# Performance work log

Hardware: AMD Instinct MI355X
Metric: run time of the kernel (lower is better)

The kernel has to match this reference:

```python
import jax, jax.numpy as jnp
import numpy as np

B, T = 32, 128
V, E, H = 32000, 512, 1024
SOS_IDX = 1


def setup_inputs() -> dict:
    key = jax.random.key(0)
    ks = jax.random.split(key, 9)
    s = lambda n: 1.0 / np.sqrt(n)
    return {
        "target": jax.random.randint(ks[0], (B, T), 0, V, dtype=jnp.int64),
        "h0": jax.random.normal(ks[1], (B, H), dtype=jnp.float32),
        "emb": jax.random.normal(ks[2], (V, E), dtype=jnp.float32),
        "W_ih": jax.random.normal(ks[3], (H, E), dtype=jnp.float32) * s(E),
        "b_ih": jax.random.normal(ks[4], (H,), dtype=jnp.float32) * s(E),
        "W_hh": jax.random.normal(ks[5], (H, H), dtype=jnp.float32) * s(H),
        "b_hh": jax.random.normal(ks[6], (H,), dtype=jnp.float32) * s(H),
        "W_out": jax.random.normal(ks[7], (V, H), dtype=jnp.float32) * s(H),
        "b_out": jax.random.normal(ks[8], (V,), dtype=jnp.float32) * s(H),
    }


def reference(target, h0, emb, W_ih, b_ih, W_hh, b_hh, W_out, b_out):
    # Teacher-forcing ratio fixed at 1.0 (deterministic): input tokens are
    # [sos, target[:,1], ..., target[:,T-1]] per the original `target[:, t+1]`.
    Bb, Tt = target.shape
    sos = jnp.full((Bb, 1), SOS_IDX, dtype=target.dtype)
    tokens = jnp.concatenate([sos, target[:, 1:]], axis=1)  # (B, T)
    x = emb[tokens]  # (B, T, E) -- embedding gather done once, vectorized

    def step(h, x_t):
        # manual RNN cell: h' = tanh(x W_ih^T + b_ih + h W_hh^T + b_hh)
        h = jnp.tanh(x_t @ W_ih.T + b_ih + h @ W_hh.T + b_hh)  # (B, H)
        out = h @ W_out.T + b_out  # (B, V) linear decode
        return h, out

    _, outs = jax.lax.scan(step, h0, jnp.swapaxes(x, 0, 1))  # (T, B, V)
    return jnp.swapaxes(outs, 0, 1)  # (B, T, V)
```

## Files before the change

kernel.cpp:

```cpp
#include <hip/hip_runtime.h>
#include <stdint.h>

#define T_SEQ 128
#define B_SZ  32
#define H_DIM 1024
#define E_DIM 512
#define V_DIM 32000
#define SOS_TOK 1
#define NCONS 224
#define NTILES 8000

typedef float v4f __attribute__((ext_vector_type(4)));
typedef short short8 __attribute__((ext_vector_type(8)));

__device__ inline uint16_t f2bf(float x) {
    uint32_t u = __float_as_uint(x);
    uint32_t r = (u + 0x7fffu + ((u >> 16) & 1u)) >> 16;
    return (uint16_t)r;
}
__device__ inline uint32_t pack2(float a, float b) {
    return (uint32_t)f2bf(a) | ((uint32_t)f2bf(b) << 16);
}

__device__ inline void gload16(const void* g, void* l) {
    __builtin_amdgcn_global_load_lds(
        (const __attribute__((address_space(1))) uint32_t*)g,
        (__attribute__((address_space(3))) uint32_t*)l, 16, 0, 0);
}

__global__ __launch_bounds__(256) void kconv(const float* __restrict__ W,
                                             uint16_t* __restrict__ Wb) {
    size_t i = ((size_t)blockIdx.x * 256 + threadIdx.x) * 8;
    float4 a = *(const float4*)&W[i];
    float4 c = *(const float4*)&W[i + 4];
    uint4 p;
    p.x = pack2(a.x, a.y); p.y = pack2(a.z, a.w);
    p.z = pack2(c.x, c.y); p.w = pack2(c.z, c.w);
    *(uint4*)&Wb[i] = p;
}

__global__ __launch_bounds__(256) void kxwm(const int* __restrict__ target,
                                            const float* __restrict__ emb,
                                            const float* __restrict__ Wih,
                                            const float* __restrict__ bih,
                                            const float* __restrict__ bhh,
                                            float* __restrict__ xW) {
    __shared__ __align__(16) uint16_t As[128 * 32];
    __shared__ __align__(16) uint16_t Bs[128 * 32];
    __shared__ int toks[128];
    int m0 = blockIdx.x * 128, n0 = blockIdx.y * 128;
    int tid = threadIdx.x;
    if (tid < 128) {
        int row = m0 + tid;
        int t = row & (T_SEQ - 1);
        toks[tid] = (t == 0) ? SOS_TOK : target[row];
    }
    __syncthreads();

    v4f acc[4][4] = {};
    int lane = tid & 63, wv = tid >> 6, wm = wv >> 1, wn = wv & 1;
    int ar = lane & 15, ko = (lane >> 4) * 8;

    for (int k0 = 0; k0 < E_DIM; k0 += 32) {
#pragma unroll
        for (int l = 0; l < 2; ++l) {
            int c = tid + l * 256;
            int r = c >> 2, ko8 = (c & 3) * 8;
            const float* asrc = &emb[(size_t)toks[r] * E_DIM + k0 + ko8];
            float4 x = *(const float4*)asrc;
            float4 y = *(const float4*)(asrc + 4);
            uint4 p;
            p.x = pack2(x.x, x.y); p.y = pack2(x.z, x.w);
            p.z = pack2(y.x, y.y); p.w = pack2(y.z, y.w);
            *(uint4*)&As[r * 32 + ko8] = p;
            const float* bsrc = &Wih[(size_t)(n0 + r) * E_DIM + k0 + ko8];
            float4 u = *(const float4*)bsrc;
            float4 v = *(const float4*)(bsrc + 4);
            uint4 q;
            q.x = pack2(u.x, u.y); q.y = pack2(u.z, u.w);
            q.z = pack2(v.x, v.y); q.w = pack2(v.z, v.w);
            *(uint4*)&Bs[r * 32 + ko8] = q;
        }
        __syncthreads();

        short8 a[4], bfr[4];
#pragma unroll
        for (int i = 0; i < 4; ++i)
            a[i] = *(const short8*)&As[(wm * 64 + i * 16 + ar) * 32 + ko];
#pragma unroll
        for (int jj = 0; jj < 4; ++jj)
            bfr[jj] = *(const short8*)&Bs[(wn * 64 + jj * 16 + ar) * 32 + ko];
#pragma unroll
        for (int i = 0; i < 4; ++i)
#pragma unroll
            for (int jj = 0; jj < 4; ++jj)
                acc[i][jj] = __builtin_amdgcn_mfma_f32_16x16x32_bf16(
                    a[i], bfr[jj], acc[i][jj], 0, 0, 0);
        __syncthreads();
    }

    int fr = lane & 15, fq = lane >> 4;
#pragma unroll
    for (int jj = 0; jj < 4; ++jj) {
        int col = n0 + wn * 64 + jj * 16 + fr;
        float bias = bih[col] + bhh[col];
#pragma unroll
        for (int i = 0; i < 4; ++i) {
            int row = m0 + wm * 64 + i * 16 + fq * 4;
#pragma unroll
            for (int q = 0; q < 4; ++q) {
                int m = row + q;
                int b = m >> 7, t = m & (T_SEQ - 1);
                xW[((size_t)t * B_SZ + b) * H_DIM + col] = acc[i][jj][q] + bias;
            }
        }
    }
}

template <bool BBF>
__global__ __launch_bounds__(256) void kfused(const uint16_t* __restrict__ hbInit,
                                              const uint16_t* __restrict__ WbHH,
                                              const float* __restrict__ xW,
                                              uint16_t* __restrict__ Hb,
                                              uint32_t* __restrict__ flags,
                                              const void* __restrict__ Bop,
                                              const float* __restrict__ bout,
                                              float* __restrict__ out) {
    __shared__ __align__(16) uint16_t As[128 * 32];
    __shared__ __align__(16) uint16_t Bs[128 * 32];
    int tid = threadIdx.x;
    int lane = tid & 63;

    if (blockIdx.x < 32) {
        __builtin_amdgcn_s_setprio(1);
        int blk = blockIdx.x;
        int bg = blk & 1, ngg = blk >> 1;
        int w = tid >> 6;
        int ncol0 = ngg * 64 + w * 16;
        int lr = lane & 15, lk = (lane >> 4) * 8;

        short8 wf[32];
        const uint16_t* wrow = WbHH + (size_t)(ncol0 + lr) * H_DIM + lk;
#pragma unroll
        for (int kt = 0; kt < 32; ++kt)
            wf[kt] = *(const short8*)(wrow + (size_t)kt * 32);

        int brow = bg * 16 + lr;
        int eb = bg * 16 + (lane >> 4) * 4;
        int en = ncol0 + lr;
        uint32_t* Hb32 = (uint32_t*)Hb;
        uint32_t* myflag = flags + (size_t)(bg * 16 + ngg) * 32;
        const uint32_t* grpflags = flags + (size_t)(bg * 16) * 32;

        for (int t = 0; t < T_SEQ; ++t) {
            const uint16_t* arow =
                ((t == 0) ? hbInit : Hb + (size_t)(t - 1) * B_SZ * H_DIM)
                + (size_t)brow * H_DIM + lk;

            float xv[4];
#pragma unroll
            for (int q = 0; q < 4; ++q)
                xv[q] = xW[((size_t)t * B_SZ + eb + q) * H_DIM + en];

            v4f ac0 = {0.f,0.f,0.f,0.f}, ac1 = {0.f,0.f,0.f,0.f};
            v4f ac2 = {0.f,0.f,0.f,0.f}, ac3 = {0.f,0.f,0.f,0.f};
            short8 af0[16], af1[16];
#pragma unroll
            for (int kt = 0; kt < 16; ++kt)
                af0[kt] = *(const short8*)(arow + (size_t)kt * 32);
#pragma unroll
            for (int kt = 0; kt < 16; ++kt)
                af1[kt] = *(const short8*)(arow + 512 + (size_t)kt * 32);
#pragma unroll
            for (int kt = 0; kt < 16; ++kt) {
                v4f* a = (kt & 3) == 0 ? &ac0 : (kt & 3) == 1 ? &ac1
                        : (kt & 3) == 2 ? &ac2 : &ac3;
                *a = __builtin_amdgcn_mfma_f32_16x16x32_bf16(af0[kt], wf[kt], *a, 0, 0, 0);
            }
#pragma unroll
            for (int kt = 0; kt < 16; ++kt) {
                v4f* a = (kt & 3) == 0 ? &ac0 : (kt & 3) == 1 ? &ac1
                        : (kt & 3) == 2 ? &ac2 : &ac3;
                *a = __builtin_amdgcn_mfma_f32_16x16x32_bf16(af1[kt], wf[16 + kt], *a, 0, 0, 0);
            }
            v4f acc = (ac0 + ac1) + (ac2 + ac3);

            float hv[4];
#pragma unroll
            for (int q = 0; q < 4; ++q)
                hv[q] = tanhf(acc[q] + xv[q]);

#pragma unroll
            for (int q = 0; q < 4; ++q) {
                float pv = __shfl_xor(hv[q], 1);
                bool mine = ((lane & 1) == 0) ? (q < 2) : (q >= 2);
                if (mine) {
                    uint32_t word = (lane & 1) ? pack2(pv, hv[q]) : pack2(hv[q], pv);
                    size_t i32 = (((size_t)t * B_SZ + eb + q) * H_DIM
                                  + (size_t)(en & ~1)) >> 1;
                    __hip_atomic_store(&Hb32[i32], word, __ATOMIC_RELAXED,
                                       __HIP_MEMORY_SCOPE_AGENT);
                }
            }

            __syncthreads();
            if (tid == 0)
                __hip_atomic_store(myflag, (uint32_t)(t + 1), __ATOMIC_RELEASE,
                                   __HIP_MEMORY_SCOPE_AGENT);
            if (t < T_SEQ - 1) {
                if (tid < 16) {
                    const uint32_t* f = grpflags + (size_t)tid * 32;
                    while (__hip_atomic_load(f, __ATOMIC_RELAXED,
                                             __HIP_MEMORY_SCOPE_AGENT) <= (uint32_t)t)
                        __builtin_amdgcn_s_sleep(2);
                }
                if (tid == 0)
                    (void)__hip_atomic_load(myflag, __ATOMIC_ACQUIRE,
                                            __HIP_MEMORY_SCOPE_AGENT);
                __syncthreads();
            }
        }
    } else {
        int c = blockIdx.x - 32;
        int wv = tid >> 6, wm = wv >> 1, wn = wv & 1;
        int ar = lane & 15, ko = (lane >> 4) * 8;
        int sx = BBF ? (((ar >> 1) & 3) << 3) : 0;
        int fr = lane & 15, fq = lane >> 4;
        int gate_seen = 0;
        const uint32_t* proxyf = flags + (size_t)(c & 31) * 32;

        const uint16_t* Bb = (const uint16_t*)Bop;
        const float*    Bf = (const float*)Bop;

        for (int g = c; g < NTILES; g += NCONS) {
            int mtp = g / 250, nt = g - mtp * 250;
            int need = 4 * mtp + 4;
            if (need > gate_seen) {
                if (tid == 0) {
                    while (__hip_atomic_load(proxyf, __ATOMIC_RELAXED,
                                             __HIP_MEMORY_SCOPE_AGENT) < (uint32_t)need)
                        __builtin_amdgcn_s_sleep(32);
                }
                __syncthreads();
                if (tid < 32) {
                    const uint32_t* f = flags + (size_t)tid * 32;
                    while (__hip_atomic_load(f, __ATOMIC_RELAXED,
                                             __HIP_MEMORY_SCOPE_AGENT) < (uint32_t)need)
                        __builtin_amdgcn_s_sleep(2);
                }
                __syncthreads();
                if (tid == 0)
                    (void)__hip_atomic_load(flags, __ATOMIC_ACQUIRE,
                                            __HIP_MEMORY_SCOPE_AGENT);
                __syncthreads();
                gate_seen = need;
            }

            int m0 = mtp * 128, n0 = nt * 128;
            v4f acc[4][4] = {};

            for (int k0 = 0; k0 < H_DIM; k0 += 32) {
                int wb = tid & ~63;
                if constexpr (BBF) {
#pragma unroll
                    for (int l = 0; l < 2; ++l) {
                        int cc = tid + l * 256;
                        int r = cc >> 2;
                        int gsw = ((cc & 3) ^ ((cc >> 3) & 3)) * 8;
                        gload16(&Hb[(size_t)(m0 + r) * H_DIM + k0 + gsw],
                                (char*)As + (size_t)(wb + l * 256) * 16);
                        gload16(&Bb[(size_t)(n0 + r) * H_DIM + k0 + gsw],
                                (char*)Bs + (size_t)(wb + l * 256) * 16);
                    }
                } else {
#pragma unroll
                    for (int l = 0; l < 2; ++l) {
                        int cc = tid + l * 256;
                        int r = cc >> 2, ko8 = (cc & 3) * 8;
                        gload16(&Hb[(size_t)(m0 + r) * H_DIM + k0 + ko8],
                                (char*)As + (size_t)(wb + l * 256) * 16);
                        const float* src = &Bf[(size_t)(n0 + r) * H_DIM + k0 + ko8];
                        float4 x = *(const float4*)src;
                        float4 y = *(const float4*)(src + 4);
                        uint4 p;
                        p.x = pack2(x.x, x.y); p.y = pack2(x.z, x.w);
                        p.z = pack2(y.x, y.y); p.w = pack2(y.z, y.w);
                        *(uint4*)&Bs[r * 32 + ko8] = p;
                    }
                }
                __syncthreads();

                short8 a[4], bfr[4];
#pragma unroll
                for (int i = 0; i < 4; ++i)
                    a[i] = *(const short8*)&As[(wm * 64 + i * 16 + ar) * 32 + (ko ^ sx)];
#pragma unroll
                for (int jj = 0; jj < 4; ++jj)
                    bfr[jj] = *(const short8*)&Bs[(wn * 64 + jj * 16 + ar) * 32 + (ko ^ sx)];
#pragma unroll
                for (int i = 0; i < 4; ++i)
#pragma unroll
                    for (int jj = 0; jj < 4; ++jj)
                        acc[i][jj] = __builtin_amdgcn_mfma_f32_16x16x32_bf16(
                            a[i], bfr[jj], acc[i][jj], 0, 0, 0);
                __syncthreads();
            }

#pragma unroll
            for (int jj = 0; jj < 4; ++jj) {
                int col = n0 + wn * 64 + jj * 16 + fr;
                float bo = bout[col];
#pragma unroll
                for (int i = 0; i < 4; ++i) {
                    int rbase = wm * 64 + i * 16 + fq * 4;
#pragma unroll
                    for (int q = 0; q < 4; ++q) {
                        int mp = m0 + rbase + q;
                        int tt = mp >> 5, bb = mp & 31;
                        out[((size_t)bb * T_SEQ + tt) * V_DIM + col] =
                            acc[i][jj][q] + bo;
                    }
                }
            }
        }
    }
}

extern "C" void kernel_launch(void* const* d_in, const int* in_sizes, int n_in,
                              void* d_out, int out_size, void* d_ws, size_t ws_size,
                              hipStream_t stream) {
    const int*   target = (const int*)d_in[0];
    const float* h0     = (const float*)d_in[1];
    const float* emb    = (const float*)d_in[2];
    const float* Wih    = (const float*)d_in[3];
    const float* bih    = (const float*)d_in[4];
    const float* Whh    = (const float*)d_in[5];
    const float* bhh    = (const float*)d_in[6];
    const float* Wout   = (const float*)d_in[7];
    const float* bout   = (const float*)d_in[8];
    float* out = (float*)d_out;

    char* ws = (char*)d_ws;
    float*    xW     = (float*)(ws);
    uint16_t* WbHH   = (uint16_t*)(ws + 16777216);
    uint16_t* hbInit = (uint16_t*)(ws + 18874368);
    uint32_t* flags  = (uint32_t*)(ws + 18939904);
    uint16_t* Hb     = (uint16_t*)(ws + 18944000);
    uint16_t* WbOut  = (uint16_t*)(ws + 27332608);
    const bool wbok = ws_size >= 92868608ull;

    kconv<<<512, 256, 0, stream>>>(Whh, WbHH);
    kconv<<<16, 256, 0, stream>>>(h0, hbInit);
    kxwm<<<dim3(32, 8), 256, 0, stream>>>(target, emb, Wih, bih, bhh, xW);
    hipMemsetAsync(flags, 0, 4096, stream);

    if (wbok) {
        kconv<<<16000, 256, 0, stream>>>(Wout, WbOut);
        kfused<true><<<32 + NCONS, 256, 0, stream>>>(hbInit, WbHH, xW, Hb, flags,
                                                     (const void*)WbOut, bout, out);
    } else {
        kfused<false><<<32 + NCONS, 256, 0, stream>>>(hbInit, WbHH, xW, Hb, flags,
                                                      (const void*)Wout, bout, out);
    }
}
```

Baseline: 1.069 ms.

## Fold weight bf16 conversions into fused kernel to overlap with recurrence

Removes the separate conversion kernels for W_hh, h0 and W_out. The recurrence blocks now convert W_hh and h0 to bf16 in registers on load, and the consumer blocks convert W_out into the workspace at kernel start, then wait on an atomic counter barrier before the output GEMM tiles. The W_out conversion can then run while the early recurrence steps execute, and fewer kernels are launched. The cost is a grid-wide spin barrier among the consumer blocks, which assumes all of them are resident at once.

```diff
diff --git a/kernel.cpp b/kernel.cpp
--- a/kernel.cpp
+++ b/kernel.cpp
@@ -9,6 +9,7 @@
 #define SOS_TOK 1
 #define NCONS 224
 #define NTILES 8000
+#define NGRAN 4096000
 
 typedef float v4f __attribute__((ext_vector_type(4)));
 typedef short short8 __attribute__((ext_vector_type(8)));
@@ -21,22 +22,19 @@
 __device__ inline uint32_t pack2(float a, float b) {
     return (uint32_t)f2bf(a) | ((uint32_t)f2bf(b) << 16);
 }
+__device__ inline short8 packf8(const float* p) {
+    float4 x = *(const float4*)p;
+    float4 y = *(const float4*)(p + 4);
+    uint4 v;
+    v.x = pack2(x.x, x.y); v.y = pack2(x.z, x.w);
+    v.z = pack2(y.x, y.y); v.w = pack2(y.z, y.w);
+    return *(short8*)&v;
+}
 
 __device__ inline void gload16(const void* g, void* l) {
     __builtin_amdgcn_global_load_lds(
         (const __attribute__((address_space(1))) uint32_t*)g,
         (__attribute__((address_space(3))) uint32_t*)l, 16, 0, 0);
-}
-
-__global__ __launch_bounds__(256) void kconv(const float* __restrict__ W,
-                                             uint16_t* __restrict__ Wb) {
-    size_t i = ((size_t)blockIdx.x * 256 + threadIdx.x) * 8;
-    float4 a = *(const float4*)&W[i];
-    float4 c = *(const float4*)&W[i + 4];
-    uint4 p;
-    p.x = pack2(a.x, a.y); p.y = pack2(a.z, a.w);
-    p.z = pack2(c.x, c.y); p.w = pack2(c.z, c.w);
-    *(uint4*)&Wb[i] = p;
 }
 
 __global__ __launch_bounds__(256) void kxwm(const int* __restrict__ target,
@@ -66,20 +64,10 @@
         for (int l = 0; l < 2; ++l) {
             int c = tid + l * 256;
             int r = c >> 2, ko8 = (c & 3) * 8;
-            const float* asrc = &emb[(size_t)toks[r] * E_DIM + k0 + ko8];
-            float4 x = *(const float4*)asrc;
-            float4 y = *(const float4*)(asrc + 4);
-            uint4 p;
-            p.x = pack2(x.x, x.y); p.y = pack2(x.z, x.w);
-            p.z = pack2(y.x, y.y); p.w = pack2(y.z, y.w);
-            *(uint4*)&As[r * 32 + ko8] = p;
-            const float* bsrc = &Wih[(size_t)(n0 + r) * E_DIM + k0 + ko8];
-            float4 u = *(const float4*)bsrc;
-            float4 v = *(const float4*)(bsrc + 4);
-            uint4 q;
-            q.x = pack2(u.x, u.y); q.y = pack2(u.z, u.w);
-            q.z = pack2(v.x, v.y); q.w = pack2(v.z, v.w);
-            *(uint4*)&Bs[r * 32 + ko8] = q;
+            short8 av = packf8(&emb[(size_t)toks[r] * E_DIM + k0 + ko8]);
+            short8 bv = packf8(&Wih[(size_t)(n0 + r) * E_DIM + k0 + ko8]);
+            *(short8*)&As[r * 32 + ko8] = av;
+            *(short8*)&Bs[r * 32 + ko8] = bv;
         }
         __syncthreads();
 
@@ -118,12 +106,14 @@
 }
 
 template <bool BBF>
-__global__ __launch_bounds__(256) void kfused(const uint16_t* __restrict__ hbInit,
-                                              const uint16_t* __restrict__ WbHH,
+__global__ __launch_bounds__(256) void kfused(const float* __restrict__ h0f,
+                                              const float* __restrict__ Whh,
                                               const float* __restrict__ xW,
                                               uint16_t* __restrict__ Hb,
                                               uint32_t* __restrict__ flags,
-                                              const void* __restrict__ Bop,
+                                              uint32_t* __restrict__ cnt,
+                                              const float* __restrict__ WoutF,
+                                              uint16_t* __restrict__ wbuf,
                                               const float* __restrict__ bout,
                                               float* __restrict__ out) {
     __shared__ __align__(16) uint16_t As[128 * 32];
@@ -140,10 +130,10 @@
         int lr = lane & 15, lk = (lane >> 4) * 8;
 
         short8 wf[32];
-        const uint16_t* wrow = WbHH + (size_t)(ncol0 + lr) * H_DIM + lk;
+        const float* wsrc = Whh + (size_t)(ncol0 + lr) * H_DIM + lk;
 #pragma unroll
         for (int kt = 0; kt < 32; ++kt)
-            wf[kt] = *(const short8*)(wrow + (size_t)kt * 32);
+            wf[kt] = packf8(wsrc + (size_t)kt * 32);
 
         int brow = bg * 16 + lr;
         int eb = bg * 16 + (lane >> 4) * 4;
@@ -153,10 +143,6 @@
         const uint32_t* grpflags = flags + (size_t)(bg * 16) * 32;
 
         for (int t = 0; t < T_SEQ; ++t) {
-            const uint16_t* arow =
-                ((t == 0) ? hbInit : Hb + (size_t)(t - 1) * B_SZ * H_DIM)
-                + (size_t)brow * H_DIM + lk;
-
             float xv[4];
 #pragma unroll
             for (int q = 0; q < 4; ++q)
@@ -165,12 +151,24 @@
             v4f ac0 = {0.f,0.f,0.f,0.f}, ac1 = {0.f,0.f,0.f,0.f};
             v4f ac2 = {0.f,0.f,0.f,0.f}, ac3 = {0.f,0.f,0.f,0.f};
             short8 af0[16], af1[16];
-#pragma unroll
-            for (int kt = 0; kt < 16; ++kt)
-                af0[kt] = *(const short8*)(arow + (size_t)kt * 32);
-#pragma unroll
-            for (int kt = 0; kt < 16; ++kt)
-                af1[kt] = *(const short8*)(arow + 512 + (size_t)kt * 32);
+            if (t == 0) {
+                const float* hrow = h0f + (size_t)brow * H_DIM + lk;
+#pragma unroll
+                for (int kt = 0; kt < 16; ++kt)
+                    af0[kt] = packf8(hrow + (size_t)kt * 32);
+#pragma unroll
+                for (int kt = 0; kt < 16; ++kt)
+                    af1[kt] = packf8(hrow + 512 + (size_t)kt * 32);
+            } else {
+                const uint16_t* arow = Hb + (size_t)(t - 1) * B_SZ * H_DIM
+                                       + (size_t)brow * H_DIM + lk;
+#pragma unroll
+                for (int kt = 0; kt < 16; ++kt)
+                    af0[kt] = *(const short8*)(arow + (size_t)kt * 32);
+#pragma unroll
+                for (int kt = 0; kt < 16; ++kt)
+                    af1[kt] = *(const short8*)(arow + 512 + (size_t)kt * 32);
+            }
 #pragma unroll
             for (int kt = 0; kt < 16; ++kt) {
                 v4f* a = (kt & 3) == 0 ? &ac0 : (kt & 3) == 1 ? &ac1
@@ -222,6 +220,30 @@
         }
     } else {
         int c = blockIdx.x - 32;
+
+        if constexpr (BBF) {
+            for (size_t idx = (size_t)c * 256 + tid; idx < (size_t)NGRAN;
+                 idx += (size_t)NCONS * 256) {
+                size_t i = idx * 8;
+                float4 a = *(const float4*)&WoutF[i];
+                float4 b = *(const float4*)&WoutF[i + 4];
+                uint4 p;
+                p.x = pack2(a.x, a.y); p.y = pack2(a.z, a.w);
+                p.z = pack2(b.x, b.y); p.w = pack2(b.z, b.w);
+                *(uint4*)&wbuf[i] = p;
+            }
+            __syncthreads();
+            if (tid == 0) {
+                __hip_atomic_fetch_add(cnt, 1u, __ATOMIC_RELEASE,
+                                       __HIP_MEMORY_SCOPE_AGENT);
+                while (__hip_atomic_load(cnt, __ATOMIC_RELAXED,
+                                         __HIP_MEMORY_SCOPE_AGENT) < (uint32_t)NCONS)
+                    __builtin_amdgcn_s_sleep(16);
+            }
+            __syncthreads();
+            __builtin_amdgcn_fence(__ATOMIC_ACQUIRE, "agent");
+        }
+
         int wv = tid >> 6, wm = wv >> 1, wn = wv & 1;
         int ar = lane & 15, ko = (lane >> 4) * 8;
         int sx = BBF ? (((ar >> 1) & 3) << 3) : 0;
@@ -229,8 +251,8 @@
         int gate_seen = 0;
         const uint32_t* proxyf = flags + (size_t)(c & 31) * 32;
 
-        const uint16_t* Bb = (const uint16_t*)Bop;
-        const float*    Bf = (const float*)Bop;
+        const uint16_t* Bb = wbuf;
+        const float*    Bf = WoutF;
 
         for (int g = c; g < NTILES; g += NCONS) {
             int mtp = g / 250, nt = g - mtp * 250;
@@ -279,13 +301,8 @@
                         int r = cc >> 2, ko8 = (cc & 3) * 8;
                         gload16(&Hb[(size_t)(m0 + r) * H_DIM + k0 + ko8],
                                 (char*)As + (size_t)(wb + l * 256) * 16);
-                        const float* src = &Bf[(size_t)(n0 + r) * H_DIM + k0 + ko8];
-                        float4 x = *(const float4*)src;
-                        float4 y = *(const float4*)(src + 4);
-                        uint4 p;
-                        p.x = pack2(x.x, x.y); p.y = pack2(x.z, x.w);
-                        p.z = pack2(y.x, y.y); p.w = pack2(y.z, y.w);
-                        *(uint4*)&Bs[r * 32 + ko8] = p;
+                        short8 pv = packf8(&Bf[(size_t)(n0 + r) * H_DIM + k0 + ko8]);
+                        *(short8*)&Bs[r * 32 + ko8] = pv;
                     }
                 }
                 __syncthreads();
@@ -342,24 +359,20 @@
 
     char* ws = (char*)d_ws;
     float*    xW     = (float*)(ws);
-    uint16_t* WbHH   = (uint16_t*)(ws + 16777216);
-    uint16_t* hbInit = (uint16_t*)(ws + 18874368);
+    uint32_t* cnt    = (uint32_t*)(ws + 18874368);
     uint32_t* flags  = (uint32_t*)(ws + 18939904);
     uint16_t* Hb     = (uint16_t*)(ws + 18944000);
     uint16_t* WbOut  = (uint16_t*)(ws + 27332608);
     const bool wbok = ws_size >= 92868608ull;
 
-    kconv<<<512, 256, 0, stream>>>(Whh, WbHH);
-    kconv<<<16, 256, 0, stream>>>(h0, hbInit);
     kxwm<<<dim3(32, 8), 256, 0, stream>>>(target, emb, Wih, bih, bhh, xW);
-    hipMemsetAsync(flags, 0, 4096, stream);
+    (void)hipMemsetAsync(ws + 18874368, 0, 69632, stream);
 
     if (wbok) {
-        kconv<<<16000, 256, 0, stream>>>(Wout, WbOut);
-        kfused<true><<<32 + NCONS, 256, 0, stream>>>(hbInit, WbHH, xW, Hb, flags,
-                                                     (const void*)WbOut, bout, out);
+        kfused<true><<<32 + NCONS, 256, 0, stream>>>(h0, Whh, xW, Hb, flags, cnt,
+                                                     Wout, WbOut, bout, out);
     } else {
-        kfused<false><<<32 + NCONS, 256, 0, stream>>>(hbInit, WbHH, xW, Hb, flags,
-                                                      (const void*)Wout, bout, out);
-    }
-}
+        kfused<false><<<32 + NCONS, 256, 0, stream>>>(h0, Whh, xW, Hb, flags, cnt,
+                                                      Wout, WbOut, bout, out);
+    }
+}
```

Measured after the change: 1.112 ms. +4.1%, slower.
